# Kernel optimization log

Hardware: AMD Instinct MI355X
Metric: run time of the kernel (lower is better)

## Reference

```python
import jax, jax.numpy as jnp
import numpy as np

B, I, H = 2048, 2048, 2048

def setup_inputs() -> dict:
    key = jax.random.key(0)
    ks = jax.random.split(key, 5)
    # Xavier-ish scale for weights
    W_ih = jax.random.normal(ks[0], (4 * H, I), jnp.float32) * (1.0 / np.sqrt(I))
    W_hh = jax.random.normal(ks[1], (4 * H, H), jnp.float32) * (1.0 / np.sqrt(H))
    b_ih = jnp.zeros((4 * H,), jnp.float32).at[H:2 * H].set(1.0)  # forget bias = 1
    b_hh = jnp.zeros((4 * H,), jnp.float32).at[H:2 * H].set(1.0)
    return {
        "x": jax.random.normal(ks[2], (B, I), jnp.float32),
        "h_prev": jax.random.normal(ks[3], (B, H), jnp.float32),
        "C_prev": jax.random.normal(ks[4], (B, H), jnp.float32),
        "W_ih": W_ih, "b_ih": b_ih, "W_hh": W_hh, "b_hh": b_hh,
    }

def reference(x, h_prev, C_prev, W_ih, b_ih, W_hh, b_hh):
    # Two GEMMs producing pre-activations for all four gates: [B, 4H]
    gates = jnp.dot(x, W_ih.T) + b_ih + jnp.dot(h_prev, W_hh.T) + b_hh
    gi, gf, gg, go = jnp.split(gates, 4, axis=1)  # torch chunk order: i, f, g, o
    input_gate = jax.nn.sigmoid(gi)
    forget_gate = jax.nn.sigmoid(gf)
    candidate_gate = jnp.tanh(gg)
    output_gate = jax.nn.sigmoid(go)
    new_C = forget_gate * C_prev + input_gate * candidate_gate
    new_h = output_gate * jnp.tanh(new_C)
    return (new_h, new_C, forget_gate, input_gate, candidate_gate, output_gate)
```

## Files before the change

kernel.cpp:

```cpp
#include <hip/hip_runtime.h>
#include <cstdint>
#include <cstddef>


typedef __attribute__((ext_vector_type(8))) short bf16x8;
typedef __attribute__((ext_vector_type(4))) float f32x4;

#define GLD_AS1 const __attribute__((address_space(1))) void
#define GLD_AS3 __attribute__((address_space(3))) void

__device__ __forceinline__ void gload_lds16(const void* g, void* l) {
  __builtin_amdgcn_global_load_lds((GLD_AS1*)g, (GLD_AS3*)l, 16, 0, 0);
}

__device__ __forceinline__ unsigned short f2bf(float f) {
  unsigned int u = __float_as_uint(f);
  unsigned int r = 0x7FFFu + ((u >> 16) & 1u);
  return (unsigned short)((u + r) >> 16);
}

__device__ __forceinline__ void barrier_f() {
  asm volatile("" ::: "memory");
  __builtin_amdgcn_s_barrier();
  asm volatile("" ::: "memory");
}

__device__ __forceinline__ float sigm(float x) { return 1.0f / (1.0f + __expf(-x)); }

__global__ __launch_bounds__(256) void cvt_all(const float* __restrict__ x,
                                               const float* __restrict__ h,
                                               const float* __restrict__ Wih,
                                               const float* __restrict__ Whh,
                                               unsigned short* __restrict__ Abf,
                                               unsigned short* __restrict__ Wbf) {
  int bid = blockIdx.x;
  const float* src; unsigned short* dst; int col_off; int base;
  if (bid < 4096)        { src = x;   dst = Abf; col_off = 0;    base = bid; }
  else if (bid < 8192)   { src = h;   dst = Abf; col_off = 2048; base = bid - 4096; }
  else if (bid < 24576)  { src = Wih; dst = Wbf; col_off = 0;    base = bid - 8192; }
  else                   { src = Whh; dst = Wbf; col_off = 2048; base = bid - 24576; }
  int i = base * 256 + threadIdx.x;
  int flat = i << 2;
  int r = flat >> 11;
  int c = flat & 2047;
  float4 v = *(const float4*)(src + flat);
  ushort4 o;
  o.x = f2bf(v.x); o.y = f2bf(v.y); o.z = f2bf(v.z); o.w = f2bf(v.w);
  *(ushort4*)(dst + (((size_t)r) << 12) + col_off + c) = o;
}

__global__ __launch_bounds__(512, 2) void gemm_lstm(
    const unsigned short* __restrict__ A,
    const unsigned short* __restrict__ W,
    const float* __restrict__ b_ih, const float* __restrict__ b_hh,
    const float* __restrict__ C_prev,
    float* __restrict__ out)
{
  constexpr int K = 4096;
  constexpr int BK = 64;
  constexpr int NT = K / BK;
  __shared__ alignas(16) unsigned short lds[2][4][128 * 64];

  int b  = blockIdx.x;
  int xc = b & 7, ii = b >> 3;
  int bm = (ii & 7) * 256;
  int h0 = (xc * 4 + (ii >> 3)) * 64;

  int tid  = threadIdx.x;
  int lane = tid & 63;
  int w    = tid >> 6;
  int wm   = w >> 2;
  int wn   = w & 3;
  int l15  = lane & 15;
  int lq   = lane >> 4;

  int ce0 = ((lq * 16) ^ ((l15 & 7) << 4)) >> 1;
  int ce1 = ((64 + lq * 16) ^ ((l15 & 7) << 4)) >> 1;

  int srow_s = lane >> 3;
  int scol = ((lane & 7) ^ (lane >> 3)) * 8;
  const unsigned short* gA = A + (size_t)(bm + 16 * w + srow_s) * K + scol;
  const unsigned short* gB0 =
      W + (size_t)((w & 3) * 2048 + h0 + 16 * (w >> 2) + srow_s) * K + scol;

  f32x4 acc[8][4] = {};

  auto stageA = [&](int t, int hh) {
    unsigned short* l0 = &lds[t & 1][hh][w * 1024];
    const unsigned short* g = gA + (size_t)hh * 128 * K + t * BK;
    gload_lds16(g, l0);
    gload_lds16(g + (size_t)8 * K, l0 + 512);
  };
  auto stageB = [&](int t, int hh) {
    unsigned short* l0 = &lds[t & 1][2 + hh][w * 1024];
    const unsigned short* g = gB0 + (size_t)hh * 32 * K + t * BK;
    gload_lds16(g, l0);
    gload_lds16(g + (size_t)8 * K, l0 + 512);
  };

  stageA(0, 0); stageA(0, 1); stageB(0, 0); stageB(0, 1);
  stageA(1, 0); stageA(1, 1); stageB(1, 0); stageB(1, 1);

  bf16x8 af[4][2], af2[4][2], bf01[2][2], bf23[2][2];

  for (int t = 0; t < NT; ++t) {
    if (t < NT - 1) asm volatile("s_waitcnt vmcnt(8)" ::: "memory");
    else            asm volatile("s_waitcnt vmcnt(0)" ::: "memory");
    barrier_f();

    const unsigned short* Ab = lds[t & 1][wm];
    const unsigned short* Bb = lds[t & 1][2 + (wn >> 1)];
    int brow = (wn & 1) * 64;

#pragma unroll
    for (int mt = 0; mt < 4; ++mt) {
      af[mt][0] = *(const bf16x8*)&Ab[(mt * 16 + l15) * 64 + ce0];
      af[mt][1] = *(const bf16x8*)&Ab[(mt * 16 + l15) * 64 + ce1];
    }
#pragma unroll
    for (int nt = 0; nt < 2; ++nt) {
      bf01[nt][0] = *(const bf16x8*)&Bb[(brow + nt * 16 + l15) * 64 + ce0];
      bf01[nt][1] = *(const bf16x8*)&Bb[(brow + nt * 16 + l15) * 64 + ce1];
    }
#pragma unroll
    for (int nt = 0; nt < 2; ++nt) {
      bf23[nt][0] = *(const bf16x8*)&Bb[(brow + (2 + nt) * 16 + l15) * 64 + ce0];
      bf23[nt][1] = *(const bf16x8*)&Bb[(brow + (2 + nt) * 16 + l15) * 64 + ce1];
    }
#pragma unroll
    for (int mt = 0; mt < 4; ++mt) {
      af2[mt][0] = *(const bf16x8*)&Ab[(64 + mt * 16 + l15) * 64 + ce0];
      af2[mt][1] = *(const bf16x8*)&Ab[(64 + mt * 16 + l15) * 64 + ce1];
    }

    __builtin_amdgcn_s_setprio(1);
#pragma unroll
    for (int mt = 0; mt < 4; ++mt)
#pragma unroll
      for (int nt = 0; nt < 2; ++nt) {
        acc[mt][nt] = __builtin_amdgcn_mfma_f32_16x16x32_bf16(af[mt][0], bf01[nt][0], acc[mt][nt], 0, 0, 0);
        acc[mt][nt] = __builtin_amdgcn_mfma_f32_16x16x32_bf16(af[mt][1], bf01[nt][1], acc[mt][nt], 0, 0, 0);
      }
#pragma unroll
    for (int mt = 0; mt < 4; ++mt)
#pragma unroll
      for (int nt = 0; nt < 2; ++nt) {
        acc[mt][2 + nt] = __builtin_amdgcn_mfma_f32_16x16x32_bf16(af[mt][0], bf23[nt][0], acc[mt][2 + nt], 0, 0, 0);
        acc[mt][2 + nt] = __builtin_amdgcn_mfma_f32_16x16x32_bf16(af[mt][1], bf23[nt][1], acc[mt][2 + nt], 0, 0, 0);
      }
    __builtin_amdgcn_s_setprio(0);

    barrier_f();
    if (t + 2 < NT) { stageB(t + 2, 0); stageB(t + 2, 1); }

    __builtin_amdgcn_s_setprio(1);
#pragma unroll
    for (int mt = 0; mt < 4; ++mt)
#pragma unroll
      for (int nt = 0; nt < 2; ++nt) {
        acc[4 + mt][2 + nt] = __builtin_amdgcn_mfma_f32_16x16x32_bf16(af2[mt][0], bf23[nt][0], acc[4 + mt][2 + nt], 0, 0, 0);
        acc[4 + mt][2 + nt] = __builtin_amdgcn_mfma_f32_16x16x32_bf16(af2[mt][1], bf23[nt][1], acc[4 + mt][2 + nt], 0, 0, 0);
      }
    __builtin_amdgcn_s_setprio(0);

    barrier_f();
    if (t + 2 < NT) { stageA(t + 2, 0); stageA(t + 2, 1); }

    __builtin_amdgcn_s_setprio(1);
#pragma unroll
    for (int mt = 0; mt < 4; ++mt)
#pragma unroll
      for (int nt = 0; nt < 2; ++nt) {
        acc[4 + mt][nt] = __builtin_amdgcn_mfma_f32_16x16x32_bf16(af2[mt][0], bf01[nt][0], acc[4 + mt][nt], 0, 0, 0);
        acc[4 + mt][nt] = __builtin_amdgcn_mfma_f32_16x16x32_bf16(af2[mt][1], bf01[nt][1], acc[4 + mt][nt], 0, 0, 0);
      }
    __builtin_amdgcn_s_setprio(0);
  }

  int hcol = h0 + wn * 16 + l15;
  float cb0 = b_ih[hcol]          + b_hh[hcol];
  float cb1 = b_ih[2048 + hcol]   + b_hh[2048 + hcol];
  float cb2 = b_ih[4096 + hcol]   + b_hh[4096 + hcol];
  float cb3 = b_ih[6144 + hcol]   + b_hh[6144 + hcol];
  constexpr size_t SEC = (size_t)2048 * 2048;
#pragma unroll
  for (int mt = 0; mt < 8; ++mt) {
    int row0 = bm + wm * 128 + mt * 16 + lq * 4;
#pragma unroll
    for (int j = 0; j < 4; ++j) {
      size_t off = (size_t)(row0 + j) * 2048 + hcol;
      float I = sigm(acc[mt][0][j] + cb0);
      float F = sigm(acc[mt][1][j] + cb1);
      float G = tanhf(acc[mt][2][j] + cb2);
      float O = sigm(acc[mt][3][j] + cb3);
      float C = F * C_prev[off] + I * G;
      float H = O * tanhf(C);
      out[0 * SEC + off] = H;
      out[1 * SEC + off] = C;
      out[2 * SEC + off] = F;
      out[3 * SEC + off] = I;
      out[4 * SEC + off] = G;
      out[5 * SEC + off] = O;
    }
  }
}

extern "C" void kernel_launch(void* const* d_in, const int* in_sizes, int n_in,
                              void* d_out, int out_size, void* d_ws, size_t ws_size,
                              hipStream_t stream) {
  const float* x   = (const float*)d_in[0];
  const float* h   = (const float*)d_in[1];
  const float* Cp  = (const float*)d_in[2];
  const float* Wih = (const float*)d_in[3];
  const float* bih = (const float*)d_in[4];
  const float* Whh = (const float*)d_in[5];
  const float* bhh = (const float*)d_in[6];
  float* out = (float*)d_out;

  uint8_t* ws = (uint8_t*)d_ws;
  unsigned short* Abf  = (unsigned short*)ws;
  unsigned short* Wbf  = (unsigned short*)(ws + (size_t)(16u << 20));

  cvt_all<<<40960, 256, 0, stream>>>(x, h, Wih, Whh, Abf, Wbf);
  gemm_lstm<<<256, 512, 0, stream>>>(Abf, Wbf, bih, bhh, Cp, out);
}
```

Baseline: 185.2 us.

## Peel last K-iteration to overlap epilogue with MFMA and prefetch C_prev

Peels the final K tile out of the main loop. C_prev and the biases are loaded before that last compute step, and the activation and store epilogue for the first half of the rows runs while the remaining MFMAs are still pending. It also replaces tanhf and the sigmoid divide with a clamped exp-based tanh and fast division, and merges several MFMA loops. This is meant to hide epilogue memory latency and shorten the math tail, at the cost of more registers (32 cached C_prev values) and slightly lower accuracy from the approximate tanh.

Measured after the change: 205.6 us. 1.11x slower.

```diff
diff --git a/kernel.cpp b/kernel.cpp
--- a/kernel.cpp
+++ b/kernel.cpp
@@ -25,7 +25,14 @@
   asm volatile("" ::: "memory");
 }
 
-__device__ __forceinline__ float sigm(float x) { return 1.0f / (1.0f + __expf(-x)); }
+__device__ __forceinline__ float sigm(float x) {
+  return __fdividef(1.0f, 1.0f + __expf(-x));
+}
+__device__ __forceinline__ float ftanh(float x) {
+  float xc = fminf(fmaxf(x, -9.0f), 9.0f);
+  float e = __expf(2.0f * xc);
+  return 1.0f - __fdividef(2.0f, e + 1.0f);
+}
 
 __global__ __launch_bounds__(256) void cvt_all(const float* __restrict__ x,
                                                const float* __restrict__ h,
@@ -98,14 +105,16 @@
     gload_lds16(g + (size_t)8 * K, l0 + 512);
   };
 
+  int hcol = h0 + wn * 16 + l15;
+  constexpr size_t SEC = (size_t)2048 * 2048;
+
   stageA(0, 0); stageA(0, 1); stageB(0, 0); stageB(0, 1);
   stageA(1, 0); stageA(1, 1); stageB(1, 0); stageB(1, 1);
 
   bf16x8 af[4][2], af2[4][2], bf01[2][2], bf23[2][2];
 
-  for (int t = 0; t < NT; ++t) {
-    if (t < NT - 1) asm volatile("s_waitcnt vmcnt(8)" ::: "memory");
-    else            asm volatile("s_waitcnt vmcnt(0)" ::: "memory");
+  for (int t = 0; t < NT - 1; ++t) {
+    asm volatile("s_waitcnt vmcnt(8)" ::: "memory");
     barrier_f();
 
     const unsigned short* Ab = lds[t & 1][wm];
@@ -121,9 +130,6 @@
     for (int nt = 0; nt < 2; ++nt) {
       bf01[nt][0] = *(const bf16x8*)&Bb[(brow + nt * 16 + l15) * 64 + ce0];
       bf01[nt][1] = *(const bf16x8*)&Bb[(brow + nt * 16 + l15) * 64 + ce1];
-    }
-#pragma unroll
-    for (int nt = 0; nt < 2; ++nt) {
       bf23[nt][0] = *(const bf16x8*)&Bb[(brow + (2 + nt) * 16 + l15) * 64 + ce0];
       bf23[nt][1] = *(const bf16x8*)&Bb[(brow + (2 + nt) * 16 + l15) * 64 + ce1];
     }
@@ -140,11 +146,6 @@
       for (int nt = 0; nt < 2; ++nt) {
         acc[mt][nt] = __builtin_amdgcn_mfma_f32_16x16x32_bf16(af[mt][0], bf01[nt][0], acc[mt][nt], 0, 0, 0);
         acc[mt][nt] = __builtin_amdgcn_mfma_f32_16x16x32_bf16(af[mt][1], bf01[nt][1], acc[mt][nt], 0, 0, 0);
-      }
-#pragma unroll
-    for (int mt = 0; mt < 4; ++mt)
-#pragma unroll
-      for (int nt = 0; nt < 2; ++nt) {
         acc[mt][2 + nt] = __builtin_amdgcn_mfma_f32_16x16x32_bf16(af[mt][0], bf23[nt][0], acc[mt][2 + nt], 0, 0, 0);
         acc[mt][2 + nt] = __builtin_amdgcn_mfma_f32_16x16x32_bf16(af[mt][1], bf23[nt][1], acc[mt][2 + nt], 0, 0, 0);
       }
@@ -177,30 +178,110 @@
     __builtin_amdgcn_s_setprio(0);
   }
 
-  int hcol = h0 + wn * 16 + l15;
-  float cb0 = b_ih[hcol]          + b_hh[hcol];
-  float cb1 = b_ih[2048 + hcol]   + b_hh[2048 + hcol];
-  float cb2 = b_ih[4096 + hcol]   + b_hh[4096 + hcol];
-  float cb3 = b_ih[6144 + hcol]   + b_hh[6144 + hcol];
-  constexpr size_t SEC = (size_t)2048 * 2048;
-#pragma unroll
-  for (int mt = 0; mt < 8; ++mt) {
-    int row0 = bm + wm * 128 + mt * 16 + lq * 4;
-#pragma unroll
-    for (int j = 0; j < 4; ++j) {
-      size_t off = (size_t)(row0 + j) * 2048 + hcol;
-      float I = sigm(acc[mt][0][j] + cb0);
-      float F = sigm(acc[mt][1][j] + cb1);
-      float G = tanhf(acc[mt][2][j] + cb2);
-      float O = sigm(acc[mt][3][j] + cb3);
-      float C = F * C_prev[off] + I * G;
-      float H = O * tanhf(C);
-      out[0 * SEC + off] = H;
-      out[1 * SEC + off] = C;
-      out[2 * SEC + off] = F;
-      out[3 * SEC + off] = I;
-      out[4 * SEC + off] = G;
-      out[5 * SEC + off] = O;
+  {
+    const int t = NT - 1;
+    asm volatile("s_waitcnt vmcnt(0)" ::: "memory");
+    barrier_f();
+
+    float cb0 = b_ih[hcol]        + b_hh[hcol];
+    float cb1 = b_ih[2048 + hcol] + b_hh[2048 + hcol];
+    float cb2 = b_ih[4096 + hcol] + b_hh[4096 + hcol];
+    float cb3 = b_ih[6144 + hcol] + b_hh[6144 + hcol];
+    float cp[32];
+#pragma unroll
+    for (int mt = 0; mt < 8; ++mt) {
+      int row0 = bm + wm * 128 + mt * 16 + lq * 4;
+#pragma unroll
+      for (int j = 0; j < 4; ++j)
+        cp[mt * 4 + j] = C_prev[(size_t)(row0 + j) * 2048 + hcol];
+    }
+
+    const unsigned short* Ab = lds[t & 1][wm];
+    const unsigned short* Bb = lds[t & 1][2 + (wn >> 1)];
+    int brow = (wn & 1) * 64;
+
+#pragma unroll
+    for (int mt = 0; mt < 4; ++mt) {
+      af[mt][0] = *(const bf16x8*)&Ab[(mt * 16 + l15) * 64 + ce0];
+      af[mt][1] = *(const bf16x8*)&Ab[(mt * 16 + l15) * 64 + ce1];
+    }
+#pragma unroll
+    for (int nt = 0; nt < 2; ++nt) {
+      bf01[nt][0] = *(const bf16x8*)&Bb[(brow + nt * 16 + l15) * 64 + ce0];
+      bf01[nt][1] = *(const bf16x8*)&Bb[(brow + nt * 16 + l15) * 64 + ce1];
+      bf23[nt][0] = *(const bf16x8*)&Bb[(brow + (2 + nt) * 16 + l15) * 64 + ce0];
+      bf23[nt][1] = *(const bf16x8*)&Bb[(brow + (2 + nt) * 16 + l15) * 64 + ce1];
+    }
+#pragma unroll
+    for (int mt = 0; mt < 4; ++mt) {
+      af2[mt][0] = *(const bf16x8*)&Ab[(64 + mt * 16 + l15) * 64 + ce0];
+      af2[mt][1] = *(const bf16x8*)&Ab[(64 + mt * 16 + l15) * 64 + ce1];
+    }
+
+    __builtin_amdgcn_s_setprio(1);
+#pragma unroll
+    for (int mt = 0; mt < 4; ++mt)
+#pragma unroll
+      for (int nt = 0; nt < 2; ++nt) {
+        acc[mt][nt] = __builtin_amdgcn_mfma_f32_16x16x32_bf16(af[mt][0], bf01[nt][0], acc[mt][nt], 0, 0, 0);
+        acc[mt][nt] = __builtin_amdgcn_mfma_f32_16x16x32_bf16(af[mt][1], bf01[nt][1], acc[mt][nt], 0, 0, 0);
+        acc[mt][2 + nt] = __builtin_amdgcn_mfma_f32_16x16x32_bf16(af[mt][0], bf23[nt][0], acc[mt][2 + nt], 0, 0, 0);
+        acc[mt][2 + nt] = __builtin_amdgcn_mfma_f32_16x16x32_bf16(af[mt][1], bf23[nt][1], acc[mt][2 + nt], 0, 0, 0);
+      }
+    __builtin_amdgcn_s_setprio(0);
+
+#pragma unroll
+    for (int mt = 0; mt < 4; ++mt) {
+      int row0 = bm + wm * 128 + mt * 16 + lq * 4;
+#pragma unroll
+      for (int j = 0; j < 4; ++j) {
+        size_t off = (size_t)(row0 + j) * 2048 + hcol;
+        float I = sigm(acc[mt][0][j] + cb0);
+        float F = sigm(acc[mt][1][j] + cb1);
+        float G = ftanh(acc[mt][2][j] + cb2);
+        float O = sigm(acc[mt][3][j] + cb3);
+        float C = F * cp[mt * 4 + j] + I * G;
+        float H = O * ftanh(C);
+        out[0 * SEC + off] = H;
+        out[1 * SEC + off] = C;
+        out[2 * SEC + off] = F;
+        out[3 * SEC + off] = I;
+        out[4 * SEC + off] = G;
+        out[5 * SEC + off] = O;
+      }
+    }
+
+    __builtin_amdgcn_s_setprio(1);
+#pragma unroll
+    for (int mt = 0; mt < 4; ++mt)
+#pragma unroll
+      for (int nt = 0; nt < 2; ++nt) {
+        acc[4 + mt][2 + nt] = __builtin_amdgcn_mfma_f32_16x16x32_bf16(af2[mt][0], bf23[nt][0], acc[4 + mt][2 + nt], 0, 0, 0);
+        acc[4 + mt][2 + nt] = __builtin_amdgcn_mfma_f32_16x16x32_bf16(af2[mt][1], bf23[nt][1], acc[4 + mt][2 + nt], 0, 0, 0);
+        acc[4 + mt][nt] = __builtin_amdgcn_mfma_f32_16x16x32_bf16(af2[mt][0], bf01[nt][0], acc[4 + mt][nt], 0, 0, 0);
+        acc[4 + mt][nt] = __builtin_amdgcn_mfma_f32_16x16x32_bf16(af2[mt][1], bf01[nt][1], acc[4 + mt][nt], 0, 0, 0);
+      }
+    __builtin_amdgcn_s_setprio(0);
+
+#pragma unroll
+    for (int mt = 4; mt < 8; ++mt) {
+      int row0 = bm + wm * 128 + mt * 16 + lq * 4;
+#pragma unroll
+      for (int j = 0; j < 4; ++j) {
+        size_t off = (size_t)(row0 + j) * 2048 + hcol;
+        float I = sigm(acc[mt][0][j] + cb0);
+        float F = sigm(acc[mt][1][j] + cb1);
+        float G = ftanh(acc[mt][2][j] + cb2);
+        float O = sigm(acc[mt][3][j] + cb3);
+        float C = F * cp[mt * 4 + j] + I * G;
+        float H = O * ftanh(C);
+        out[0 * SEC + off] = H;
+        out[1 * SEC + off] = C;
+        out[2 * SEC + off] = F;
+        out[3 * SEC + off] = I;
+        out[4 * SEC + off] = G;
+        out[5 * SEC + off] = O;
+      }
     }
   }
 }
```

## Shrink GEMM tile to 128x256 with BK=32 and use fast tanh/sigmoid

Applied to the files above, without the earlier changes.

Halves the block M-tile (256→128) and K-step (64→32), doubling the grid to 512 blocks. It simplifies the LDS layout and staging into a single per-stage load and raises launch bounds to 4 blocks per CU, aiming for better occupancy and load balance across CUs. The epilogue swaps tanhf for an exp-based approximation and uses fast division. In exchange, the smaller tile lowers arithmetic intensity, adds more barriers per K-step, and slightly reduces tanh accuracy.

Measured after the change: 200.3 us. +8.2%, slower.

```diff
diff --git a/kernel.cpp b/kernel.cpp
--- a/kernel.cpp
+++ b/kernel.cpp
@@ -25,7 +25,14 @@
   asm volatile("" ::: "memory");
 }
 
-__device__ __forceinline__ float sigm(float x) { return 1.0f / (1.0f + __expf(-x)); }
+__device__ __forceinline__ float sigm(float x) {
+  return __fdividef(1.0f, 1.0f + __expf(-x));
+}
+__device__ __forceinline__ float ftanh(float x) {
+  float xc = fminf(fmaxf(x, -9.0f), 9.0f);
+  float e = __expf(2.0f * xc);
+  return 1.0f - __fdividef(2.0f, e + 1.0f);
+}
 
 __global__ __launch_bounds__(256) void cvt_all(const float* __restrict__ x,
                                                const float* __restrict__ h,
@@ -49,7 +56,7 @@
   *(ushort4*)(dst + (((size_t)r) << 12) + col_off + c) = o;
 }
 
-__global__ __launch_bounds__(512, 2) void gemm_lstm(
+__global__ __launch_bounds__(512, 4) void gemm_lstm(
     const unsigned short* __restrict__ A,
     const unsigned short* __restrict__ W,
     const float* __restrict__ b_ih, const float* __restrict__ b_hh,
@@ -57,14 +64,14 @@
     float* __restrict__ out)
 {
   constexpr int K = 4096;
-  constexpr int BK = 64;
+  constexpr int BK = 32;
   constexpr int NT = K / BK;
-  __shared__ alignas(16) unsigned short lds[2][4][128 * 64];
+  __shared__ alignas(16) unsigned short lds[2][(128 + 256) * 32];
 
   int b  = blockIdx.x;
   int xc = b & 7, ii = b >> 3;
-  int bm = (ii & 7) * 256;
-  int h0 = (xc * 4 + (ii >> 3)) * 64;
+  int bm = (ii & 15) * 128;
+  int h0 = (xc * 4 + (ii >> 4)) * 64;
 
   int tid  = threadIdx.x;
   int lane = tid & 63;
@@ -74,127 +81,75 @@
   int l15  = lane & 15;
   int lq   = lane >> 4;
 
-  int ce0 = ((lq * 16) ^ ((l15 & 7) << 4)) >> 1;
-  int ce1 = ((64 + lq * 16) ^ ((l15 & 7) << 4)) >> 1;
+  int ce = (lq ^ ((l15 >> 1) & 3)) * 8;
 
-  int srow_s = lane >> 3;
-  int scol = ((lane & 7) ^ (lane >> 3)) * 8;
-  const unsigned short* gA = A + (size_t)(bm + 16 * w + srow_s) * K + scol;
+  int sr = lane >> 2;
+  int scol = ((lane & 3) ^ ((sr >> 1) & 3)) * 8;
+
+  const unsigned short* gA = A + (size_t)(bm + 16 * w + sr) * K + scol;
   const unsigned short* gB0 =
-      W + (size_t)((w & 3) * 2048 + h0 + 16 * (w >> 2) + srow_s) * K + scol;
+      W + (size_t)((2 * (w & 1)) * 2048 + h0 + 16 * (w >> 1) + sr) * K + scol;
+  const unsigned short* gB1 = gB0 + (size_t)2048 * K;
 
-  f32x4 acc[8][4] = {};
+  f32x4 acc[4][4] = {};
 
-  auto stageA = [&](int t, int hh) {
-    unsigned short* l0 = &lds[t & 1][hh][w * 1024];
-    const unsigned short* g = gA + (size_t)hh * 128 * K + t * BK;
-    gload_lds16(g, l0);
-    gload_lds16(g + (size_t)8 * K, l0 + 512);
-  };
-  auto stageB = [&](int t, int hh) {
-    unsigned short* l0 = &lds[t & 1][2 + hh][w * 1024];
-    const unsigned short* g = gB0 + (size_t)hh * 32 * K + t * BK;
-    gload_lds16(g, l0);
-    gload_lds16(g + (size_t)8 * K, l0 + 512);
+  auto stage = [&](int t) {
+    unsigned short* base = lds[t & 1];
+    int k0 = t * BK;
+    gload_lds16(gA + k0, base + w * 512 + 8 * lane);
+    gload_lds16(gB0 + k0, base + 4096 + (32 * w) * 32 + 8 * lane);
+    gload_lds16(gB1 + k0, base + 4096 + (32 * w + 16) * 32 + 8 * lane);
   };
 
-  stageA(0, 0); stageA(0, 1); stageB(0, 0); stageB(0, 1);
-  stageA(1, 0); stageA(1, 1); stageB(1, 0); stageB(1, 1);
+  stage(0); stage(1);
 
-  bf16x8 af[4][2], af2[4][2], bf01[2][2], bf23[2][2];
+  bf16x8 af[4], bg[4];
 
   for (int t = 0; t < NT; ++t) {
-    if (t < NT - 1) asm volatile("s_waitcnt vmcnt(8)" ::: "memory");
+    if (t < NT - 1) asm volatile("s_waitcnt vmcnt(3)" ::: "memory");
     else            asm volatile("s_waitcnt vmcnt(0)" ::: "memory");
     barrier_f();
 
-    const unsigned short* Ab = lds[t & 1][wm];
-    const unsigned short* Bb = lds[t & 1][2 + (wn >> 1)];
-    int brow = (wn & 1) * 64;
+    const unsigned short* Ab = lds[t & 1];
+    const unsigned short* Bb = lds[t & 1] + 4096;
 
 #pragma unroll
-    for (int mt = 0; mt < 4; ++mt) {
-      af[mt][0] = *(const bf16x8*)&Ab[(mt * 16 + l15) * 64 + ce0];
-      af[mt][1] = *(const bf16x8*)&Ab[(mt * 16 + l15) * 64 + ce1];
-    }
+    for (int mt = 0; mt < 4; ++mt)
+      af[mt] = *(const bf16x8*)&Ab[(wm * 64 + mt * 16 + l15) * 32 + ce];
 #pragma unroll
-    for (int nt = 0; nt < 2; ++nt) {
-      bf01[nt][0] = *(const bf16x8*)&Bb[(brow + nt * 16 + l15) * 64 + ce0];
-      bf01[nt][1] = *(const bf16x8*)&Bb[(brow + nt * 16 + l15) * 64 + ce1];
-    }
-#pragma unroll
-    for (int nt = 0; nt < 2; ++nt) {
-      bf23[nt][0] = *(const bf16x8*)&Bb[(brow + (2 + nt) * 16 + l15) * 64 + ce0];
-      bf23[nt][1] = *(const bf16x8*)&Bb[(brow + (2 + nt) * 16 + l15) * 64 + ce1];
-    }
-#pragma unroll
-    for (int mt = 0; mt < 4; ++mt) {
-      af2[mt][0] = *(const bf16x8*)&Ab[(64 + mt * 16 + l15) * 64 + ce0];
-      af2[mt][1] = *(const bf16x8*)&Ab[(64 + mt * 16 + l15) * 64 + ce1];
-    }
+    for (int g = 0; g < 4; ++g)
+      bg[g] = *(const bf16x8*)&Bb[(wn * 64 + g * 16 + l15) * 32 + ce];
 
     __builtin_amdgcn_s_setprio(1);
 #pragma unroll
     for (int mt = 0; mt < 4; ++mt)
 #pragma unroll
-      for (int nt = 0; nt < 2; ++nt) {
-        acc[mt][nt] = __builtin_amdgcn_mfma_f32_16x16x32_bf16(af[mt][0], bf01[nt][0], acc[mt][nt], 0, 0, 0);
-        acc[mt][nt] = __builtin_amdgcn_mfma_f32_16x16x32_bf16(af[mt][1], bf01[nt][1], acc[mt][nt], 0, 0, 0);
-      }
-#pragma unroll
-    for (int mt = 0; mt < 4; ++mt)
-#pragma unroll
-      for (int nt = 0; nt < 2; ++nt) {
-        acc[mt][2 + nt] = __builtin_amdgcn_mfma_f32_16x16x32_bf16(af[mt][0], bf23[nt][0], acc[mt][2 + nt], 0, 0, 0);
-        acc[mt][2 + nt] = __builtin_amdgcn_mfma_f32_16x16x32_bf16(af[mt][1], bf23[nt][1], acc[mt][2 + nt], 0, 0, 0);
-      }
+      for (int g = 0; g < 4; ++g)
+        acc[mt][g] = __builtin_amdgcn_mfma_f32_16x16x32_bf16(af[mt], bg[g], acc[mt][g], 0, 0, 0);
     __builtin_amdgcn_s_setprio(0);
 
     barrier_f();
-    if (t + 2 < NT) { stageB(t + 2, 0); stageB(t + 2, 1); }
-
-    __builtin_amdgcn_s_setprio(1);
-#pragma unroll
-    for (int mt = 0; mt < 4; ++mt)
-#pragma unroll
-      for (int nt = 0; nt < 2; ++nt) {
-        acc[4 + mt][2 + nt] = __builtin_amdgcn_mfma_f32_16x16x32_bf16(af2[mt][0], bf23[nt][0], acc[4 + mt][2 + nt], 0, 0, 0);
-        acc[4 + mt][2 + nt] = __builtin_amdgcn_mfma_f32_16x16x32_bf16(af2[mt][1], bf23[nt][1], acc[4 + mt][2 + nt], 0, 0, 0);
-      }
-    __builtin_amdgcn_s_setprio(0);
-
-    barrier_f();
-    if (t + 2 < NT) { stageA(t + 2, 0); stageA(t + 2, 1); }
-
-    __builtin_amdgcn_s_setprio(1);
-#pragma unroll
-    for (int mt = 0; mt < 4; ++mt)
-#pragma unroll
-      for (int nt = 0; nt < 2; ++nt) {
-        acc[4 + mt][nt] = __builtin_amdgcn_mfma_f32_16x16x32_bf16(af2[mt][0], bf01[nt][0], acc[4 + mt][nt], 0, 0, 0);
-        acc[4 + mt][nt] = __builtin_amdgcn_mfma_f32_16x16x32_bf16(af2[mt][1], bf01[nt][1], acc[4 + mt][nt], 0, 0, 0);
-      }
-    __builtin_amdgcn_s_setprio(0);
+    if (t + 2 < NT) stage(t + 2);
   }
 
   int hcol = h0 + wn * 16 + l15;
-  float cb0 = b_ih[hcol]          + b_hh[hcol];
-  float cb1 = b_ih[2048 + hcol]   + b_hh[2048 + hcol];
-  float cb2 = b_ih[4096 + hcol]   + b_hh[4096 + hcol];
-  float cb3 = b_ih[6144 + hcol]   + b_hh[6144 + hcol];
+  float cb0 = b_ih[hcol]        + b_hh[hcol];
+  float cb1 = b_ih[2048 + hcol] + b_hh[2048 + hcol];
+  float cb2 = b_ih[4096 + hcol] + b_hh[4096 + hcol];
+  float cb3 = b_ih[6144 + hcol] + b_hh[6144 + hcol];
   constexpr size_t SEC = (size_t)2048 * 2048;
 #pragma unroll
-  for (int mt = 0; mt < 8; ++mt) {
-    int row0 = bm + wm * 128 + mt * 16 + lq * 4;
+  for (int mt = 0; mt < 4; ++mt) {
+    int row0 = bm + wm * 64 + mt * 16 + lq * 4;
 #pragma unroll
     for (int j = 0; j < 4; ++j) {
       size_t off = (size_t)(row0 + j) * 2048 + hcol;
       float I = sigm(acc[mt][0][j] + cb0);
       float F = sigm(acc[mt][1][j] + cb1);
-      float G = tanhf(acc[mt][2][j] + cb2);
+      float G = ftanh(acc[mt][2][j] + cb2);
       float O = sigm(acc[mt][3][j] + cb3);
       float C = F * C_prev[off] + I * G;
-      float H = O * tanhf(C);
+      float H = O * ftanh(C);
       out[0 * SEC + off] = H;
       out[1 * SEC + off] = C;
       out[2 * SEC + off] = F;
@@ -222,5 +177,5 @@
   unsigned short* Wbf  = (unsigned short*)(ws + (size_t)(16u << 20));
 
   cvt_all<<<40960, 256, 0, stream>>>(x, h, Wih, Whh, Abf, Wbf);
-  gemm_lstm<<<256, 512, 0, stream>>>(Abf, Wbf, bih, bhh, Cp, out);
+  gemm_lstm<<<512, 512, 0, stream>>>(Abf, Wbf, bih, bhh, Cp, out);
 }
```
